# Kernel tuning notes

Hardware: AMD Instinct MI355X
Metric: run time of the kernel (lower is better)

## Reference

```python
import jax, jax.numpy as jnp
import numpy as np

N = 50000      # nodes
E = 800000     # edges
D = 128        # in = out features (required by Euler residual update)
GRID_SIZE = 5
K = 3          # spline order
GRID_LO, GRID_HI = -1.0, 1.0
EPSILON = 0.001
NUM_BASES = GRID_SIZE + K  # 8


def make_grid(in_features):
    # extended uniform grid: [in, grid_size + 2k + 1]
    h = (GRID_HI - GRID_LO) / GRID_SIZE
    g = jnp.arange(-K, GRID_SIZE + K + 1, dtype=jnp.float32) * h + GRID_LO
    return jnp.broadcast_to(g, (in_features, g.shape[0]))


def b_splines(x, grid):
    # x: [N, in]; grid: [in, g+2k+1] -> bases: [N, in, g+k] (Cox-de Boor)
    xe = x[..., None]
    bases = ((xe >= grid[:, :-1]) & (xe < grid[:, 1:])).astype(x.dtype)
    for j in range(1, K + 1):
        left = (xe - grid[:, : -(j + 1)]) / (grid[:, j:-1] - grid[:, : -(j + 1)])
        right = (grid[:, j + 1:] - xe) / (grid[:, j + 1:] - grid[:, 1:-j])
        bases = left * bases[..., :-1] + right * bases[..., 1:]
    return bases


def kan_transform(x, base_w, spline_w, grid):
    # efficient-KAN layer (scale_and_bias=False): silu base branch + spline branch
    base = jax.nn.silu(x) @ base_w.T                    # [N, out]
    sb = b_splines(x, grid)                             # [N, in, g+k]
    spl = jnp.einsum('nib,oib->no', sb, spline_w)       # [N, out]
    return base + spl


def gcn_norm_coeffs(edge_index, n):
    # A_hat symmetric normalization: deg includes self-loop (+1)
    src, dst = edge_index[0], edge_index[1]
    deg = jnp.zeros((n,), jnp.float32).at[dst].add(1.0) + 1.0
    dis = jax.lax.rsqrt(deg)
    return dis[src] * dis[dst]


def setup_inputs() -> dict:
    key = jax.random.key(0)
    ks = jax.random.split(key, 6)
    x = jax.random.uniform(ks[0], (N, D), jnp.float32) * 2.0 - 1.0  # in grid_range
    edge_index = jax.random.randint(ks[1], (2, E), 0, N, dtype=jnp.int64)
    base_w_l = jax.random.normal(ks[2], (D, D), jnp.float32) * (1.0 / np.sqrt(D))
    spline_w_l = jax.random.normal(ks[3], (D, D, NUM_BASES), jnp.float32) * 0.1
    base_w_c = jax.random.normal(ks[4], (D, D), jnp.float32) * (1.0 / np.sqrt(D))
    spline_w_c = jax.random.normal(ks[5], (D, D, NUM_BASES), jnp.float32) * 0.1
    return {"x": x, "edge_index": edge_index, "base_w_l": base_w_l,
            "spline_w_l": spline_w_l, "base_w_c": base_w_c,
            "spline_w_c": spline_w_c, "delta_t": 2}


def reference(x, edge_index, base_w_l, spline_w_l, base_w_c, spline_w_c, delta_t):
    grid = make_grid(D)
    src, dst = edge_index[0], edge_index[1]
    norm = gcn_norm_coeffs(edge_index, N)  # [E]

    def layer(h):
        # KANLayer branch on node features
        h_l = kan_transform(h, base_w_l, spline_w_l, grid)
        # KANConv branch: aggregate_first -> normalized scatter-add, then KAN
        msgs = norm[:, None] * h[src]                              # [E, D]
        agg = jax.ops.segment_sum(msgs, dst, num_segments=N)       # [N, D]
        h_c = kan_transform(agg, base_w_c, spline_w_c, grid)
        return h_l + h_c

    for _ in range(int(delta_t)):   # explicit Euler ODE steps
        x = x + EPSILON * layer(x)
    return x
```

## Files before the change

kernel.cpp:

```cpp
#include <hip/hip_runtime.h>
#include <hip/hip_bf16.h>

#define NNODES 50000
#define NEDGES 800000
#define DF 128
#define KW 1152
#define EPS 0.001f
#define NB 196

typedef __bf16 bf16x8 __attribute__((ext_vector_type(8)));
typedef __bf16 bf16x4 __attribute__((ext_vector_type(4)));
typedef float  f32x4  __attribute__((ext_vector_type(4)));
typedef unsigned long ulongx2 __attribute__((ext_vector_type(2)));

#define GLOAD16(g, l) __builtin_amdgcn_global_load_lds( \
    (const __attribute__((address_space(1))) unsigned int*)(g), \
    (__attribute__((address_space(3))) unsigned int*)(l), 16, 0, 0)

__global__ void build_wt(const float* __restrict__ bwl, const float* __restrict__ swl,
                         const float* __restrict__ bwc, const float* __restrict__ swc,
                         __bf16* __restrict__ wtl, __bf16* __restrict__ wtc) {
    int gid = blockIdx.x * 256 + threadIdx.x;
    const float* bw = blockIdx.y ? bwc : bwl;
    const float* sw = blockIdx.y ? swc : swl;
    __bf16*      wt = blockIdx.y ? wtc : wtl;
    int o = gid / KW;
    int k = gid - o * KW;
    float v = (k < 128) ? bw[o * DF + k] : sw[o * 1024 + (k - 128)];
    wt[gid] = (__bf16)v;
}

__global__ void cast_x(const float* __restrict__ x, __bf16* __restrict__ xb) {
    int i = blockIdx.x * 256 + threadIdx.x;
    f32x4 a = ((const f32x4*)x)[2 * i];
    f32x4 b = ((const f32x4*)x)[2 * i + 1];
    bf16x8 o;
    o[0] = (__bf16)a[0]; o[1] = (__bf16)a[1]; o[2] = (__bf16)a[2]; o[3] = (__bf16)a[3];
    o[4] = (__bf16)b[0]; o[5] = (__bf16)b[1]; o[6] = (__bf16)b[2]; o[7] = (__bf16)b[3];
    ((bf16x8*)xb)[i] = o;
}

__global__ void deg_count(const int* __restrict__ ei, int* __restrict__ deg) {
    int e = blockIdx.x * 256 + threadIdx.x;
    if (e >= NEDGES) return;
    atomicAdd(&deg[ei[NEDGES + e]], 1);
}

__global__ void scan_part(const int* __restrict__ deg, int* __restrict__ bsum) {
    __shared__ int red[256];
    int t = threadIdx.x;
    int i = blockIdx.x * 256 + t;
    red[t] = (i < NNODES) ? deg[i] : 0;
    __syncthreads();
    for (int off = 128; off > 0; off >>= 1) {
        if (t < off) red[t] += red[t + off];
        __syncthreads();
    }
    if (t == 0) bsum[blockIdx.x] = red[0];
}

__global__ void scan_bsum(const int* __restrict__ bsum, int* __restrict__ boff) {
    __shared__ int buf[256];
    int t = threadIdx.x;
    int v = (t < NB) ? bsum[t] : 0;
    buf[t] = v;
    __syncthreads();
    for (int off = 1; off < 256; off <<= 1) {
        int x = (t >= off) ? buf[t - off] : 0;
        __syncthreads();
        buf[t] += x;
        __syncthreads();
    }
    if (t <= NB) boff[t] = buf[t] - ((t < NB) ? bsum[t] : 0);
}

__global__ void scan_final(const int* __restrict__ deg, const int* __restrict__ boff,
                           int* __restrict__ rowptr) {
    __shared__ int buf[256];
    int t = threadIdx.x;
    int i = blockIdx.x * 256 + t;
    int v = (i < NNODES) ? deg[i] : 0;
    buf[t] = v;
    __syncthreads();
    for (int off = 1; off < 256; off <<= 1) {
        int x = (t >= off) ? buf[t - off] : 0;
        __syncthreads();
        buf[t] += x;
        __syncthreads();
    }
    if (i < NNODES) rowptr[i] = buf[t] - v + boff[blockIdx.x];
    if (blockIdx.x == 0 && t == 0) rowptr[NNODES] = boff[NB];
}

__global__ void fill_csr(const int* __restrict__ ei, const int* __restrict__ deg,
                         const int* __restrict__ rowptr, int* __restrict__ cnt,
                         int* __restrict__ esrc, float* __restrict__ ew) {
    int e = blockIdx.x * 256 + threadIdx.x;
    if (e >= NEDGES) return;
    int s = ei[e];
    int d = ei[NEDGES + e];
    float w = rsqrtf((float)(deg[s] + 1)) * rsqrtf((float)(deg[d] + 1));
    int p = rowptr[d] + atomicAdd(&cnt[d], 1);
    esrc[p] = s;
    ew[p] = w;
}

__global__ __launch_bounds__(256) void agg_gather(
        const int* __restrict__ rowptr, const int* __restrict__ esrc,
        const float* __restrict__ ew, const __bf16* __restrict__ hb,
        __bf16* __restrict__ aggb) {
    const int tid = blockIdx.x * 256 + threadIdx.x;
    const int n = tid >> 4;
    const int l = tid & 15;
    if (n >= NNODES) return;
    int p  = rowptr[n];
    const int pe = rowptr[n + 1];
    float acc[8] = {};
    int   cs0, cs1, cs2, cs3;
    float cw0, cw1, cw2, cw3;
    bool have = (p + 3 < pe);
    if (have) {
        cs0 = esrc[p]; cs1 = esrc[p + 1]; cs2 = esrc[p + 2]; cs3 = esrc[p + 3];
        cw0 = ew[p];   cw1 = ew[p + 1];   cw2 = ew[p + 2];   cw3 = ew[p + 3];
    }
    while (have) {
        int np = p + 4;
        bool nh = (np + 3 < pe);
        int   ns0 = 0, ns1 = 0, ns2 = 0, ns3 = 0;
        float nw0 = 0, nw1 = 0, nw2 = 0, nw3 = 0;
        if (nh) {
            ns0 = esrc[np]; ns1 = esrc[np + 1]; ns2 = esrc[np + 2]; ns3 = esrc[np + 3];
            nw0 = ew[np];   nw1 = ew[np + 1];   nw2 = ew[np + 2];   nw3 = ew[np + 3];
        }
        bf16x8 v0 = *(const bf16x8*)(hb + (size_t)cs0 * DF + l * 8);
        bf16x8 v1 = *(const bf16x8*)(hb + (size_t)cs1 * DF + l * 8);
        bf16x8 v2 = *(const bf16x8*)(hb + (size_t)cs2 * DF + l * 8);
        bf16x8 v3 = *(const bf16x8*)(hb + (size_t)cs3 * DF + l * 8);
#pragma unroll
        for (int j = 0; j < 8; ++j)
            acc[j] += cw0 * (float)v0[j] + cw1 * (float)v1[j]
                    + cw2 * (float)v2[j] + cw3 * (float)v3[j];
        p = np;
        cs0 = ns0; cs1 = ns1; cs2 = ns2; cs3 = ns3;
        cw0 = nw0; cw1 = nw1; cw2 = nw2; cw3 = nw3;
        have = nh;
    }
    for (; p < pe; ++p) {
        int   s0 = esrc[p];
        float w0 = ew[p];
        bf16x8 v0 = *(const bf16x8*)(hb + (size_t)s0 * DF + l * 8);
#pragma unroll
        for (int j = 0; j < 8; ++j) acc[j] += w0 * (float)v0[j];
    }
    bf16x8 o;
#pragma unroll
    for (int j = 0; j < 8; ++j) o[j] = (__bf16)acc[j];
    *(bf16x8*)(aggb + (size_t)n * DF + l * 8) = o;
}

__global__ __launch_bounds__(256, 4) void kan_step(
        const float* __restrict__ h,
        const __bf16* __restrict__ xb,
        const __bf16* __restrict__ aggb,
        const __bf16* __restrict__ wtl, const __bf16* __restrict__ wtc,
        float* __restrict__ out, __bf16* __restrict__ outb) {
    __shared__ __bf16 Bs[3][128 * 32];
    __shared__ __bf16 Xs[64 * 128];

    const int tid  = threadIdx.x;
    const int lane = tid & 63;
    const int w    = tid >> 6;
    const int q    = lane >> 4, l15 = lane & 15;
    const int n0   = blockIdx.x * 64;
    const int myrow = w * 16 + l15;
    const int msw   = myrow & 7;

    const int relrow = lane >> 2;
    const int slotx  = (lane & 3) ^ (relrow & 3);
    const int r0 = w * 16 + relrow;
    const size_t gb0 = (size_t)r0 * KW + (size_t)slotx * 8;
    const size_t gb1 = gb0 + (size_t)64 * KW;

    const int bslot = (q ^ (l15 & 3)) * 8;

    const int xrow = tid >> 2, xseg = tid & 3;
    const bool xok = (n0 + xrow) < NNODES;
    const size_t xgoff = (size_t)(n0 + xrow) * DF + xseg * 32;

    f32x4 acc[8] = {};

    auto xs_write = [&](uint4 v0, uint4 v1, uint4 v2, uint4 v3) {
        const int gl = xrow * 16 + xseg * 4;
        const int sw = xrow & 7;
        *(uint4*)&Xs[(size_t)((gl + 0) ^ sw) * 8] = v0;
        *(uint4*)&Xs[(size_t)((gl + 1) ^ sw) * 8] = v1;
        *(uint4*)&Xs[(size_t)((gl + 2) ^ sw) * 8] = v2;
        *(uint4*)&Xs[(size_t)((gl + 3) ^ sw) * 8] = v3;
    };

    auto stageB = [&](int t2, int sb) {
        const __bf16* wtp = (t2 >= 36) ? wtc : wtl;
        const int k0 = ((t2 >= 36) ? t2 - 36 : t2) * 32;
        GLOAD16(wtp + gb0 + k0, &Bs[sb][(w * 16) * 32]);
        GLOAD16(wtp + gb1 + k0, &Bs[sb][(64 + w * 16) * 32]);
    };

    auto spline_pack = [&](float x) -> bf16x8 {
        float f  = __builtin_fmaf(x, 2.5f, 5.5f);
        float fi = floorf(f);
        int  idx = (int)fi;
        float u  = f - fi;
        float u2 = u * u, u3 = u2 * u;
        float om = 1.0f - u;
        float Wa = u3 * (1.0f / 6.0f);
        float Wb = (((-3.0f * u + 3.0f) * u + 3.0f) * u + 1.0f) * (1.0f / 6.0f);
        float Wc = ((3.0f * u - 6.0f) * u2 + 4.0f) * (1.0f / 6.0f);
        float Wd = om * om * om * (1.0f / 6.0f);
        unsigned long p =
              (unsigned long)__builtin_bit_cast(unsigned short, (__bf16)Wd)
            | ((unsigned long)__builtin_bit_cast(unsigned short, (__bf16)Wc) << 16)
            | ((unsigned long)__builtin_bit_cast(unsigned short, (__bf16)Wb) << 32)
            | ((unsigned long)__builtin_bit_cast(unsigned short, (__bf16)Wa) << 48);
        int tt = idx - 3;
        unsigned long lo, hi;
        if (tt >= 0) {
            int s = (tt & 3) * 16;
            unsigned long sv = p << s;
            unsigned long cr = (p >> (63 - s)) >> 1;
            bool hh = tt >= 4;
            lo = hh ? 0ul : sv;
            hi = hh ? sv : cr;
            if (tt >= 8) { lo = 0; hi = 0; }
        } else {
            int s = (-tt) * 16;
            lo = (tt >= -3) ? (p >> (s & 63)) : 0ul;
            hi = 0;
        }
        ulongx2 r; r[0] = lo; r[1] = hi;
        return __builtin_bit_cast(bf16x8, r);
    };

    auto silu8 = [&](const __bf16* xs) -> bf16x8 {
        bf16x8 v = *(const bf16x8*)xs;
        bf16x8 o;
#pragma unroll
        for (int j = 0; j < 8; ++j) {
            float x = (float)v[j];
            o[j] = (__bf16)(x / (1.0f + __expf(-x)));
        }
        return o;
    };

    uint4 a0 = {}, a1 = {}, a2 = {}, a3 = {};
    uint4 c0 = {}, c1 = {}, c2 = {}, c3 = {};
    if (xok) {
        const uint4* ga = (const uint4*)(xb + xgoff);
        a0 = ga[0]; a1 = ga[1]; a2 = ga[2]; a3 = ga[3];
        const uint4* gc = (const uint4*)(aggb + xgoff);
        c0 = gc[0]; c1 = gc[1]; c2 = gc[2]; c3 = gc[3];
    }
    xs_write(a0, a1, a2, a3);
    stageB(0, 0);
    stageB(1, 1);
    asm volatile("s_waitcnt lgkmcnt(0)" ::: "memory");

    auto body = [&](int t, int cb, int sb, bool doStage, bool last) {
        if (last) asm volatile("s_waitcnt vmcnt(0)" ::: "memory");
        else      asm volatile("s_waitcnt vmcnt(2)" ::: "memory");
        __builtin_amdgcn_s_barrier();
        __builtin_amdgcn_sched_barrier(0);

        if (t == 36) {
            xs_write(c0, c1, c2, c3);
            asm volatile("s_waitcnt lgkmcnt(0)" ::: "memory");
            __builtin_amdgcn_s_barrier();
            __builtin_amdgcn_sched_barrier(0);
        }

        if (doStage) stageB(t + 2, sb);

        const int ck = (t >= 36) ? t - 36 : t;
        bf16x8 a;
        if (ck < 4) {
            const int g = (myrow * 16 + ck * 4 + q) ^ msw;
            a = silu8(&Xs[(size_t)g * 8]);
        } else {
            const int f = (ck - 4) * 4 + q;
            const int g = (myrow * 16 + (f >> 3)) ^ msw;
            unsigned short u0 =
                *(const unsigned short*)&Xs[(size_t)g * 8 + (f & 7)];
            a = spline_pack(__builtin_bit_cast(float, (unsigned)u0 << 16));
        }

        bf16x8 bF[8];
#pragma unroll
        for (int nj = 0; nj < 8; ++nj)
            bF[nj] = *(const bf16x8*)&Bs[cb][(nj * 16 + l15) * 32 + bslot];
#pragma unroll
        for (int nj = 0; nj < 8; ++nj)
            acc[nj] = __builtin_amdgcn_mfma_f32_16x16x32_bf16(a, bF[nj], acc[nj], 0, 0, 0);
    };

    int cb = 0, sb = 2;
#pragma unroll 3
    for (int t = 0; t < 69; ++t) {
        body(t, cb, sb, true, false);
        cb = (cb == 2) ? 0 : cb + 1;
        sb = (sb == 2) ? 0 : sb + 1;
    }
    body(69, 0, 2, true,  false);
    body(70, 1, 0, false, false);
    body(71, 2, 0, false, true);

#pragma unroll
    for (int nj = 0; nj < 8; ++nj) {
#pragma unroll
        for (int r = 0; r < 4; ++r) {
            int row = n0 + w * 16 + q * 4 + r;
            int col = nj * 16 + l15;
            if (row < NNODES) {
                size_t idx = (size_t)row * DF + col;
                float v = h[idx] + EPS * acc[nj][r];
                out[idx]  = v;
                outb[idx] = (__bf16)v;
            }
        }
    }
}

extern "C" void kernel_launch(void* const* d_in, const int* in_sizes, int n_in,
                              void* d_out, int out_size, void* d_ws, size_t ws_size,
                              hipStream_t stream) {
    const float* x   = (const float*)d_in[0];
    const int*   ei  = (const int*)d_in[1];
    const float* bwl = (const float*)d_in[2];
    const float* swl = (const float*)d_in[3];
    const float* bwc = (const float*)d_in[4];
    const float* swc = (const float*)d_in[5];
    float* out = (float*)d_out;

    char* ws = (char*)d_ws;
    int*    deg    = (int*)  (ws + 0);
    int*    cnt    = (int*)  (ws + 200000);
    int*    rowptr = (int*)  (ws + 400000);
    int*    bsum   = (int*)  (ws + 600064);
    int*    boff   = (int*)  (ws + 600896);
    int*    esrc   = (int*)  (ws + 601728);
    float*  ew     = (float*)(ws + 3801728);
    __bf16* xb     = (__bf16*)(ws + 7001728);
    __bf16* aggb   = (__bf16*)(ws + 19801728);
    __bf16* wtl    = (__bf16*)(ws + 32601728);
    __bf16* wtc    = (__bf16*)(ws + 32896640);

    build_wt<<<dim3((DF * KW) / 256, 2), 256, 0, stream>>>(bwl, swl, bwc, swc, wtl, wtc);
    cast_x<<<3125, 256, 0, stream>>>(x, xb);

    hipMemsetAsync(deg, 0, 400000, stream);
    deg_count<<<3125, 256, 0, stream>>>(ei, deg);
    scan_part<<<NB, 256, 0, stream>>>(deg, bsum);
    scan_bsum<<<1, 256, 0, stream>>>(bsum, boff);
    scan_final<<<NB, 256, 0, stream>>>(deg, boff, rowptr);
    fill_csr<<<3125, 256, 0, stream>>>(ei, deg, rowptr, cnt, esrc, ew);

    const int gemm_grid = (NNODES + 63) / 64;
    const float* h = x;
    for (int step = 0; step < 2; ++step) {
        agg_gather<<<3125, 256, 0, stream>>>(rowptr, esrc, ew, xb, aggb);
        kan_step<<<gemm_grid, 256, 0, stream>>>(h, xb, aggb, wtl, wtc, out, xb);
        h = out;
    }
}
```

Measured before the change: 381.7 us.

## Use two-wave blocks with 32-row per-wave tiles in kan_step GEMM

Changes kan_step from 4 waves at 16 rows each to 2 waves at 32 rows each, so every wave issues two MFMA chains that share the same B fragments from LDS. This halves B-fragment LDS reads per MFMA and removes the B swizzle. Each wave now stages four global-to-LDS B loads per step, and the silu/spline A computation is interleaved after the B reads. The cost is fewer waves per block for hiding latency, twice the accumulator registers, and a possible return of LDS bank conflicts now that the swizzle is gone.

After: 435.3 us. 1.14x slower.

```diff
diff --git a/kernel.cpp b/kernel.cpp
--- a/kernel.cpp
+++ b/kernel.cpp
@@ -158,7 +158,7 @@
     *(bf16x8*)(aggb + (size_t)n * DF + l * 8) = o;
 }
 
-__global__ __launch_bounds__(256, 4) void kan_step(
+__global__ __launch_bounds__(128, 2) void kan_step(
         const float* __restrict__ h,
         const __bf16* __restrict__ xb,
         const __bf16* __restrict__ aggb,
@@ -172,37 +172,32 @@
     const int w    = tid >> 6;
     const int q    = lane >> 4, l15 = lane & 15;
     const int n0   = blockIdx.x * 64;
-    const int myrow = w * 16 + l15;
-    const int msw   = myrow & 7;
-
-    const int relrow = lane >> 2;
-    const int slotx  = (lane & 3) ^ (relrow & 3);
-    const int r0 = w * 16 + relrow;
-    const size_t gb0 = (size_t)r0 * KW + (size_t)slotx * 8;
-    const size_t gb1 = gb0 + (size_t)64 * KW;
-
-    const int bslot = (q ^ (l15 & 3)) * 8;
-
-    const int xrow = tid >> 2, xseg = tid & 3;
+    const int row0 = w * 32 + l15;
+    const int msw  = row0 & 7;
+
+    const size_t gbBase = (size_t)(w * 64 + (lane >> 2)) * KW + (size_t)(lane & 3) * 8;
+
+    const int xrow = tid >> 1, xseg = tid & 1;
     const bool xok = (n0 + xrow) < NNODES;
-    const size_t xgoff = (size_t)(n0 + xrow) * DF + xseg * 32;
-
-    f32x4 acc[8] = {};
-
-    auto xs_write = [&](uint4 v0, uint4 v1, uint4 v2, uint4 v3) {
-        const int gl = xrow * 16 + xseg * 4;
+    const size_t xgoff = (size_t)(n0 + xrow) * DF + xseg * 64;
+
+    f32x4 acc0[8] = {}, acc1[8] = {};
+
+    auto xs_write = [&](const uint4 (&v)[8]) {
+        const int gl = xrow * 16 + xseg * 8;
         const int sw = xrow & 7;
-        *(uint4*)&Xs[(size_t)((gl + 0) ^ sw) * 8] = v0;
-        *(uint4*)&Xs[(size_t)((gl + 1) ^ sw) * 8] = v1;
-        *(uint4*)&Xs[(size_t)((gl + 2) ^ sw) * 8] = v2;
-        *(uint4*)&Xs[(size_t)((gl + 3) ^ sw) * 8] = v3;
+#pragma unroll
+        for (int i = 0; i < 8; ++i)
+            *(uint4*)&Xs[(size_t)((gl + i) ^ sw) * 8] = v[i];
     };
 
     auto stageB = [&](int t2, int sb) {
         const __bf16* wtp = (t2 >= 36) ? wtc : wtl;
         const int k0 = ((t2 >= 36) ? t2 - 36 : t2) * 32;
-        GLOAD16(wtp + gb0 + k0, &Bs[sb][(w * 16) * 32]);
-        GLOAD16(wtp + gb1 + k0, &Bs[sb][(64 + w * 16) * 32]);
+#pragma unroll
+        for (int j = 0; j < 4; ++j)
+            GLOAD16(wtp + gbBase + (size_t)(j * 16) * KW + k0,
+                    &Bs[sb][(w * 64 + j * 16) * 32]);
     };
 
     auto spline_pack = [&](float x) -> bf16x8 {
@@ -240,8 +235,7 @@
         return __builtin_bit_cast(bf16x8, r);
     };
 
-    auto silu8 = [&](const __bf16* xs) -> bf16x8 {
-        bf16x8 v = *(const bf16x8*)xs;
+    auto silu8v = [&](bf16x8 v) -> bf16x8 {
         bf16x8 o;
 #pragma unroll
         for (int j = 0; j < 8; ++j) {
@@ -251,27 +245,26 @@
         return o;
     };
 
-    uint4 a0 = {}, a1 = {}, a2 = {}, a3 = {};
-    uint4 c0 = {}, c1 = {}, c2 = {}, c3 = {};
+    uint4 a[8] = {}, c[8] = {};
     if (xok) {
         const uint4* ga = (const uint4*)(xb + xgoff);
-        a0 = ga[0]; a1 = ga[1]; a2 = ga[2]; a3 = ga[3];
         const uint4* gc = (const uint4*)(aggb + xgoff);
-        c0 = gc[0]; c1 = gc[1]; c2 = gc[2]; c3 = gc[3];
-    }
-    xs_write(a0, a1, a2, a3);
+#pragma unroll
+        for (int i = 0; i < 8; ++i) { a[i] = ga[i]; c[i] = gc[i]; }
+    }
+    xs_write(a);
     stageB(0, 0);
     stageB(1, 1);
     asm volatile("s_waitcnt lgkmcnt(0)" ::: "memory");
 
     auto body = [&](int t, int cb, int sb, bool doStage, bool last) {
         if (last) asm volatile("s_waitcnt vmcnt(0)" ::: "memory");
-        else      asm volatile("s_waitcnt vmcnt(2)" ::: "memory");
+        else      asm volatile("s_waitcnt vmcnt(4)" ::: "memory");
         __builtin_amdgcn_s_barrier();
         __builtin_amdgcn_sched_barrier(0);
 
         if (t == 36) {
-            xs_write(c0, c1, c2, c3);
+            xs_write(c);
             asm volatile("s_waitcnt lgkmcnt(0)" ::: "memory");
             __builtin_amdgcn_s_barrier();
             __builtin_amdgcn_sched_barrier(0);
@@ -280,25 +273,37 @@
         if (doStage) stageB(t + 2, sb);
 
         const int ck = (t >= 36) ? t - 36 : t;
-        bf16x8 a;
+        bf16x8 xv0, xv1;
+        unsigned short s0 = 0, s1 = 0;
         if (ck < 4) {
-            const int g = (myrow * 16 + ck * 4 + q) ^ msw;
-            a = silu8(&Xs[(size_t)g * 8]);
+            const int g0 = (row0 * 16 + ck * 4 + q) ^ msw;
+            const int g1 = ((row0 + 16) * 16 + ck * 4 + q) ^ msw;
+            xv0 = *(const bf16x8*)&Xs[(size_t)g0 * 8];
+            xv1 = *(const bf16x8*)&Xs[(size_t)g1 * 8];
         } else {
-            const int f = (ck - 4) * 4 + q;
-            const int g = (myrow * 16 + (f >> 3)) ^ msw;
-            unsigned short u0 =
-                *(const unsigned short*)&Xs[(size_t)g * 8 + (f & 7)];
-            a = spline_pack(__builtin_bit_cast(float, (unsigned)u0 << 16));
-        }
-
+            const int f  = (ck - 4) * 4 + q;
+            const int g0 = (row0 * 16 + (f >> 3)) ^ msw;
+            const int g1 = ((row0 + 16) * 16 + (f >> 3)) ^ msw;
+            s0 = *(const unsigned short*)&Xs[(size_t)g0 * 8 + (f & 7)];
+            s1 = *(const unsigned short*)&Xs[(size_t)g1 * 8 + (f & 7)];
+        }
         bf16x8 bF[8];
 #pragma unroll
         for (int nj = 0; nj < 8; ++nj)
-            bF[nj] = *(const bf16x8*)&Bs[cb][(nj * 16 + l15) * 32 + bslot];
-#pragma unroll
-        for (int nj = 0; nj < 8; ++nj)
-            acc[nj] = __builtin_amdgcn_mfma_f32_16x16x32_bf16(a, bF[nj], acc[nj], 0, 0, 0);
+            bF[nj] = *(const bf16x8*)&Bs[cb][(nj * 16 + l15) * 32 + q * 8];
+        bf16x8 a0, a1;
+        if (ck < 4) {
+            a0 = silu8v(xv0);
+            a1 = silu8v(xv1);
+        } else {
+            a0 = spline_pack(__builtin_bit_cast(float, (unsigned)s0 << 16));
+            a1 = spline_pack(__builtin_bit_cast(float, (unsigned)s1 << 16));
+        }
+#pragma unroll
+        for (int nj = 0; nj < 8; ++nj) {
+            acc0[nj] = __builtin_amdgcn_mfma_f32_16x16x32_bf16(a0, bF[nj], acc0[nj], 0, 0, 0);
+            acc1[nj] = __builtin_amdgcn_mfma_f32_16x16x32_bf16(a1, bF[nj], acc1[nj], 0, 0, 0);
+        }
     };
 
     int cb = 0, sb = 2;
@@ -316,11 +321,18 @@
     for (int nj = 0; nj < 8; ++nj) {
 #pragma unroll
         for (int r = 0; r < 4; ++r) {
-            int row = n0 + w * 16 + q * 4 + r;
-            int col = nj * 16 + l15;
+            const int col = nj * 16 + l15;
+            int row = n0 + w * 32 + q * 4 + r;
             if (row < NNODES) {
                 size_t idx = (size_t)row * DF + col;
-                float v = h[idx] + EPS * acc[nj][r];
+                float v = h[idx] + EPS * acc0[nj][r];
+                out[idx]  = v;
+                outb[idx] = (__bf16)v;
+            }
+            row += 16;
+            if (row < NNODES) {
+                size_t idx = (size_t)row * DF + col;
+                float v = h[idx] + EPS * acc1[nj][r];
                 out[idx]  = v;
                 outb[idx] = (__bf16)v;
             }
@@ -366,7 +378,7 @@
     const float* h = x;
     for (int step = 0; step < 2; ++step) {
         agg_gather<<<3125, 256, 0, stream>>>(rowptr, esrc, ew, xb, aggb);
-        kan_step<<<gemm_grid, 256, 0, stream>>>(h, xb, aggb, wtl, wtc, out, xb);
+        kan_step<<<gemm_grid, 128, 0, stream>>>(h, xb, aggb, wtl, wtc, out, xb);
         h = out;
     }
 }
```

## Pre-swizzle weights into MFMA fragment order and load B directly to registers

Applied to the files above, without the earlier changes.

The weight matrices are repacked once into a layout that matches the MFMA B-fragment lane order, so the GEMM kernel reads B operands straight from global memory into registers with a double-buffered register prefetch. This removes the LDS staging ring, the global_load_lds instructions and the per-step block barriers. Launch bounds drop to 3 waves per SIMD to make room for the extra register buffers. The cost is that every block re-reads the weights through L2/L1 rather than sharing them in LDS, and global load latency is hidden only by a one-step prefetch distance.

After: 414.6 us. 8.6% more time.

```diff
diff --git a/kernel.cpp b/kernel.cpp
--- a/kernel.cpp
+++ b/kernel.cpp
@@ -13,21 +13,23 @@
 typedef float  f32x4  __attribute__((ext_vector_type(4)));
 typedef unsigned long ulongx2 __attribute__((ext_vector_type(2)));
 
-#define GLOAD16(g, l) __builtin_amdgcn_global_load_lds( \
-    (const __attribute__((address_space(1))) unsigned int*)(g), \
-    (__attribute__((address_space(3))) unsigned int*)(l), 16, 0, 0)
-
 __global__ void build_wt(const float* __restrict__ bwl, const float* __restrict__ swl,
                          const float* __restrict__ bwc, const float* __restrict__ swc,
-                         __bf16* __restrict__ wtl, __bf16* __restrict__ wtc) {
-    int gid = blockIdx.x * 256 + threadIdx.x;
-    const float* bw = blockIdx.y ? bwc : bwl;
-    const float* sw = blockIdx.y ? swc : swl;
-    __bf16*      wt = blockIdx.y ? wtc : wtl;
-    int o = gid / KW;
-    int k = gid - o * KW;
-    float v = (k < 128) ? bw[o * DF + k] : sw[o * 1024 + (k - 128)];
-    wt[gid] = (__bf16)v;
+                         __bf16* __restrict__ wtf) {
+    int idx = blockIdx.x * 256 + threadIdx.x;
+    int j    = idx & 7;
+    int lane = (idx >> 3) & 63;
+    int nj   = (idx >> 9) & 7;
+    int t    = idx >> 12;
+    int l15 = lane & 15, q = lane >> 4;
+    int bc = (t >= 36);
+    int ck = bc ? t - 36 : t;
+    const float* bw = bc ? bwc : bwl;
+    const float* sw = bc ? swc : swl;
+    int row = nj * 16 + l15;
+    int k = ck * 32 + q * 8 + j;
+    float v = (k < 128) ? bw[row * DF + k] : sw[row * 1024 + (k - 128)];
+    wtf[idx] = (__bf16)v;
 }
 
 __global__ void cast_x(const float* __restrict__ x, __bf16* __restrict__ xb) {
@@ -158,13 +160,12 @@
     *(bf16x8*)(aggb + (size_t)n * DF + l * 8) = o;
 }
 
-__global__ __launch_bounds__(256, 4) void kan_step(
+__global__ __launch_bounds__(256, 3) void kan_step(
         const float* __restrict__ h,
         const __bf16* __restrict__ xb,
         const __bf16* __restrict__ aggb,
-        const __bf16* __restrict__ wtl, const __bf16* __restrict__ wtc,
+        const __bf16* __restrict__ wtf,
         float* __restrict__ out, __bf16* __restrict__ outb) {
-    __shared__ __bf16 Bs[3][128 * 32];
     __shared__ __bf16 Xs[64 * 128];
 
     const int tid  = threadIdx.x;
@@ -175,17 +176,11 @@
     const int myrow = w * 16 + l15;
     const int msw   = myrow & 7;
 
-    const int relrow = lane >> 2;
-    const int slotx  = (lane & 3) ^ (relrow & 3);
-    const int r0 = w * 16 + relrow;
-    const size_t gb0 = (size_t)r0 * KW + (size_t)slotx * 8;
-    const size_t gb1 = gb0 + (size_t)64 * KW;
-
-    const int bslot = (q ^ (l15 & 3)) * 8;
-
     const int xrow = tid >> 2, xseg = tid & 3;
     const bool xok = (n0 + xrow) < NNODES;
     const size_t xgoff = (size_t)(n0 + xrow) * DF + xseg * 32;
+
+    const __bf16* fbase = wtf + (size_t)lane * 8;
 
     f32x4 acc[8] = {};
 
@@ -198,11 +193,11 @@
         *(uint4*)&Xs[(size_t)((gl + 3) ^ sw) * 8] = v3;
     };
 
-    auto stageB = [&](int t2, int sb) {
-        const __bf16* wtp = (t2 >= 36) ? wtc : wtl;
-        const int k0 = ((t2 >= 36) ? t2 - 36 : t2) * 32;
-        GLOAD16(wtp + gb0 + k0, &Bs[sb][(w * 16) * 32]);
-        GLOAD16(wtp + gb1 + k0, &Bs[sb][(64 + w * 16) * 32]);
+    auto loadF = [&](bf16x8 (&bX)[8], int t) {
+        const __bf16* fb = fbase + (size_t)t * 4096;
+#pragma unroll
+        for (int nj = 0; nj < 8; ++nj)
+            bX[nj] = *(const bf16x8*)(fb + nj * 512);
     };
 
     auto spline_pack = [&](float x) -> bf16x8 {
@@ -251,34 +246,7 @@
         return o;
     };
 
-    uint4 a0 = {}, a1 = {}, a2 = {}, a3 = {};
-    uint4 c0 = {}, c1 = {}, c2 = {}, c3 = {};
-    if (xok) {
-        const uint4* ga = (const uint4*)(xb + xgoff);
-        a0 = ga[0]; a1 = ga[1]; a2 = ga[2]; a3 = ga[3];
-        const uint4* gc = (const uint4*)(aggb + xgoff);
-        c0 = gc[0]; c1 = gc[1]; c2 = gc[2]; c3 = gc[3];
-    }
-    xs_write(a0, a1, a2, a3);
-    stageB(0, 0);
-    stageB(1, 1);
-    asm volatile("s_waitcnt lgkmcnt(0)" ::: "memory");
-
-    auto body = [&](int t, int cb, int sb, bool doStage, bool last) {
-        if (last) asm volatile("s_waitcnt vmcnt(0)" ::: "memory");
-        else      asm volatile("s_waitcnt vmcnt(2)" ::: "memory");
-        __builtin_amdgcn_s_barrier();
-        __builtin_amdgcn_sched_barrier(0);
-
-        if (t == 36) {
-            xs_write(c0, c1, c2, c3);
-            asm volatile("s_waitcnt lgkmcnt(0)" ::: "memory");
-            __builtin_amdgcn_s_barrier();
-            __builtin_amdgcn_sched_barrier(0);
-        }
-
-        if (doStage) stageB(t + 2, sb);
-
+    auto compute = [&](int t, const bf16x8 (&bF)[8]) {
         const int ck = (t >= 36) ? t - 36 : t;
         bf16x8 a;
         if (ck < 4) {
@@ -291,26 +259,38 @@
                 *(const unsigned short*)&Xs[(size_t)g * 8 + (f & 7)];
             a = spline_pack(__builtin_bit_cast(float, (unsigned)u0 << 16));
         }
-
-        bf16x8 bF[8];
-#pragma unroll
-        for (int nj = 0; nj < 8; ++nj)
-            bF[nj] = *(const bf16x8*)&Bs[cb][(nj * 16 + l15) * 32 + bslot];
 #pragma unroll
         for (int nj = 0; nj < 8; ++nj)
             acc[nj] = __builtin_amdgcn_mfma_f32_16x16x32_bf16(a, bF[nj], acc[nj], 0, 0, 0);
     };
 
-    int cb = 0, sb = 2;
-#pragma unroll 3
-    for (int t = 0; t < 69; ++t) {
-        body(t, cb, sb, true, false);
-        cb = (cb == 2) ? 0 : cb + 1;
-        sb = (sb == 2) ? 0 : sb + 1;
-    }
-    body(69, 0, 2, true,  false);
-    body(70, 1, 0, false, false);
-    body(71, 2, 0, false, true);
+    uint4 a0 = {}, a1 = {}, a2 = {}, a3 = {};
+    uint4 c0 = {}, c1 = {}, c2 = {}, c3 = {};
+    if (xok) {
+        const uint4* ga = (const uint4*)(xb + xgoff);
+        a0 = ga[0]; a1 = ga[1]; a2 = ga[2]; a3 = ga[3];
+        const uint4* gc = (const uint4*)(aggb + xgoff);
+        c0 = gc[0]; c1 = gc[1]; c2 = gc[2]; c3 = gc[3];
+    }
+    xs_write(a0, a1, a2, a3);
+    asm volatile("s_waitcnt lgkmcnt(0)" ::: "memory");
+
+    bf16x8 bA[8], bB[8];
+    loadF(bA, 0);
+    loadF(bB, 1);
+
+    for (int t = 0; t < 70; t += 2) {
+        if (t == 36) {
+            xs_write(c0, c1, c2, c3);
+            asm volatile("s_waitcnt lgkmcnt(0)" ::: "memory");
+        }
+        compute(t, bA);
+        loadF(bA, t + 2);
+        compute(t + 1, bB);
+        if (t + 3 < 72) loadF(bB, t + 3);
+    }
+    compute(70, bA);
+    compute(71, bB);
 
 #pragma unroll
     for (int nj = 0; nj < 8; ++nj) {
@@ -349,10 +329,9 @@
     float*  ew     = (float*)(ws + 3801728);
     __bf16* xb     = (__bf16*)(ws + 7001728);
     __bf16* aggb   = (__bf16*)(ws + 19801728);
-    __bf16* wtl    = (__bf16*)(ws + 32601728);
-    __bf16* wtc    = (__bf16*)(ws + 32896640);
-
-    build_wt<<<dim3((DF * KW) / 256, 2), 256, 0, stream>>>(bwl, swl, bwc, swc, wtl, wtc);
+    __bf16* wtf    = (__bf16*)(ws + 32601728);
+
+    build_wt<<<1152, 256, 0, stream>>>(bwl, swl, bwc, swc, wtf);
     cast_x<<<3125, 256, 0, stream>>>(x, xb);
 
     hipMemsetAsync(deg, 0, 400000, stream);
@@ -366,7 +345,7 @@
     const float* h = x;
     for (int step = 0; step < 2; ++step) {
         agg_gather<<<3125, 256, 0, stream>>>(rowptr, esrc, ew, xb, aggb);
-        kan_step<<<gemm_grid, 256, 0, stream>>>(h, xb, aggb, wtl, wtc, out, xb);
+        kan_step<<<gemm_grid, 256, 0, stream>>>(h, xb, aggb, wtf, out, xb);
         h = out;
     }
 }
```
